# Optimization experiments

Measured on AMD Instinct MI355X. Metric: run time of the kernel, lower is better.

Reference implementation:

```python
import math
import jax, jax.numpy as jnp
import numpy as np

B, S, D = 4, 2048, 1280
H, HD = 16, 80  # num_heads, head_dim
LOG2E = 1.442695041


def setup_inputs() -> dict:
    key = jax.random.key(0)
    ks = jax.random.split(key, 6)
    hidden_states = jax.random.normal(ks[0], (B, S, D), dtype=jnp.float32)
    # additive causal mask: 0 on/below diagonal, large negative above
    causal = jnp.tril(jnp.ones((S, S), dtype=bool))
    attention_mask = jnp.where(causal, 0.0, -1e9).astype(jnp.float32)[None, None, :, :]
    attention_mask = jnp.broadcast_to(attention_mask, (B, 1, S, S))
    scaling = jax.random.normal(ks[1], (HD,), dtype=jnp.float32)
    fan = 1.0 / math.sqrt(D)
    qkv_w = jax.random.normal(ks[2], (3 * H * HD, D), dtype=jnp.float32) * fan
    qkv_b = jax.random.normal(ks[3], (3 * H * HD,), dtype=jnp.float32) * fan
    o_w = jax.random.normal(ks[4], (D, H * HD), dtype=jnp.float32) * (1.0 / math.sqrt(H * HD))
    o_b = jax.random.normal(ks[5], (D,), dtype=jnp.float32) * fan
    return {
        "hidden_states": hidden_states,
        "attention_mask": attention_mask,
        "scaling": scaling,
        "qkv_w": qkv_w,
        "qkv_b": qkv_b,
        "o_w": o_w,
        "o_b": o_b,
    }


def reference(hidden_states, attention_mask, scaling, qkv_w, qkv_b, o_w, o_b):
    b, s, _ = hidden_states.shape
    qkv = hidden_states @ qkv_w.T + qkv_b  # [b, s, 3*H*HD]
    xq, xk, xv = jnp.split(qkv, [H * HD, 2 * H * HD], axis=-1)
    xq = xq.reshape(b, s, H, HD)
    xk = xk.reshape(b, s, H, HD)
    xv = xv.reshape(b, s, H, HD)
    # per-dim query scaling: softplus(scaling) * log2(e) / sqrt(head_dim)
    scale = jax.nn.softplus(scaling) * (LOG2E / math.sqrt(HD))
    xq = xq * scale[None, None, None, :]
    scores = jnp.einsum("bqhd,bkhd->bhqk", xq, xk) + attention_mask  # [b,H,s,s]
    probs = jax.nn.softmax(scores.astype(jnp.float32), axis=-1).astype(xq.dtype)
    out = jnp.einsum("bhqk,bkhd->bqhd", probs, xv).reshape(b, s, H * HD)
    return out @ o_w.T + o_b
```

## Files before the change

kernel.cpp:

```cpp
#include <hip/hip_runtime.h>
#include <math.h>

#define B_ 4
#define S_ 2048
#define D_ 1280
#define H_ 16
#define HD_ 80
#define HHD (H_ * HD_)
#define QKVN (3 * H_ * HD_)

typedef __bf16 bf16x8 __attribute__((ext_vector_type(8)));
typedef __bf16 bf16x4 __attribute__((ext_vector_type(4)));
typedef float  f32x4  __attribute__((ext_vector_type(4)));

__global__ __launch_bounds__(256) void cvt_all(
    const float* __restrict__ h,  __bf16* __restrict__ hb,
    const float* __restrict__ qw, __bf16* __restrict__ qwb,
    const float* __restrict__ ow, __bf16* __restrict__ owb)
{
    const int n0 = (B_ * S_ * D_) / 8;
    const int n1 = (QKVN * D_) / 8;
    const int g = blockIdx.x * 256 + threadIdx.x;

    const float* in;
    __bf16* out;
    int i;
    if (g < n0)            { in = h;  out = hb;  i = g; }
    else if (g < n0 + n1)  { in = qw; out = qwb; i = g - n0; }
    else                   { in = ow; out = owb; i = g - n0 - n1; }

    const float4 a = ((const float4*)in)[2 * (size_t)i];
    const float4 b = ((const float4*)in)[2 * (size_t)i + 1];
    bf16x8 v = {(__bf16)a.x, (__bf16)a.y, (__bf16)a.z, (__bf16)a.w,
                (__bf16)b.x, (__bf16)b.y, (__bf16)b.z, (__bf16)b.w};
    *(bf16x8*)(out + 8 * (size_t)i) = v;
}

__device__ __forceinline__ void async_copy16(const void* g, void* l)
{
    __builtin_amdgcn_global_load_lds(
        (const __attribute__((address_space(1))) unsigned int*)g,
        (__attribute__((address_space(3))) unsigned int*)l, 16, 0, 0);
}

__device__ __forceinline__ bf16x8 frag_ld(const char* lds, int m, int j)
{
    return *(const bf16x8*)(lds + m * 128 + ((j ^ (m & 7)) << 4));
}

__device__ __forceinline__ void stage_half256(
    const __bf16* __restrict__ src, int K, char* ldsmat, int half, int tid)
{
    const int wave = tid >> 6, lane = tid & 63;
#pragma unroll
    for (int i = 0; i < 2; ++i) {
        const int c = (i * 8 + wave) * 64 + lane;
        const int r = half * 128 + (c >> 3);
        const int g = (c & 7) ^ (r & 7);
        async_copy16(src + (size_t)r * K + g * 8,
                     ldsmat + half * 16384 + (i * 8 + wave) * 1024);
    }
}

#define QBAR() do { asm volatile("" ::: "memory");                             \
                    __builtin_amdgcn_s_barrier();                              \
                    __builtin_amdgcn_sched_barrier(0); } while (0)

#define RD_A(MH)                                                               \
    _Pragma("unroll")                                                          \
    for (int mi = 0; mi < 4; ++mi)                                             \
        _Pragma("unroll")                                                      \
        for (int ks = 0; ks < 2; ++ks)                                         \
            af[mi][ks] = frag_ld(lA, wm * 128 + (MH) * 64 + mi * 16 + l16,     \
                                 ks * 4 + quad);
#define RD_B(NH)                                                               \
    _Pragma("unroll")                                                          \
    for (int ni = 0; ni < 2; ++ni)                                             \
        _Pragma("unroll")                                                      \
        for (int ks = 0; ks < 2; ++ks)                                         \
            bfr[ni][ks] = frag_ld(lB, wn * 64 + (NH) * 32 + ni * 16 + l16,     \
                                  ks * 4 + quad);
#define MM16(MH, NH)                                                           \
    __builtin_amdgcn_s_setprio(1);                                             \
    _Pragma("unroll")                                                          \
    for (int mi = 0; mi < 4; ++mi)                                             \
        _Pragma("unroll")                                                      \
        for (int ni = 0; ni < 2; ++ni) {                                       \
            acc[(MH)*4+mi][(NH)*2+ni] = __builtin_amdgcn_mfma_f32_16x16x32_bf16( \
                af[mi][0], bfr[ni][0], acc[(MH)*4+mi][(NH)*2+ni], 0, 0, 0);    \
            acc[(MH)*4+mi][(NH)*2+ni] = __builtin_amdgcn_mfma_f32_16x16x32_bf16( \
                af[mi][1], bfr[ni][1], acc[(MH)*4+mi][(NH)*2+ni], 0, 0, 0);    \
        }                                                                      \
    __builtin_amdgcn_s_setprio(0);

#define GEMM256_PIPELINE(A_, W_)                                               \
    stage_half256(A_, D_, lds[0][0], 0, tid);                                  \
    stage_half256(A_, D_, lds[0][0], 1, tid);                                  \
    stage_half256(W_, D_, lds[0][1], 0, tid);                                  \
    stage_half256(W_, D_, lds[0][1], 1, tid);                                  \
    for (int t = 0; t < nt; ++t) {                                             \
        const int cur = t & 1;                                                 \
        const char* lA = lds[cur][0];                                          \
        const char* lB = lds[cur][1];                                          \
        char* sA = lds[cur ^ 1][0];                                            \
        char* sB = lds[cur ^ 1][1];                                            \
        const int kn = (t + 1 < nt ? t + 1 : t) * 64;                          \
                     \
        stage_half256(A_ + kn, D_, sA, 0, tid);                                \
        asm volatile("s_waitcnt vmcnt(2)" ::: "memory");                       \
        QBAR();                                                                \
        RD_A(0) RD_B(0) MM16(0, 0)                                             \
        stage_half256(A_ + kn, D_, sA, 1, tid);                                \
        RD_B(1) MM16(0, 1)                                                     \
        stage_half256(W_ + kn, D_, sB, 0, tid);                                \
        RD_A(1) RD_B(0) MM16(1, 0)                                             \
        stage_half256(W_ + kn, D_, sB, 1, tid);                                \
        RD_B(1) MM16(1, 1)                                                     \
        QBAR();                                                                \
    }

__global__ __launch_bounds__(512, 2) void gemm_qkv_256(
    const __bf16* __restrict__ Ab, const __bf16* __restrict__ Wb,
    const float* __restrict__ bias, const float* __restrict__ scaling,
    __bf16* __restrict__ Qb, __bf16* __restrict__ Kb, __bf16* __restrict__ Vtb)
{
    __shared__ __align__(16) char lds[2][2][32768];
    const int tid = threadIdx.x;
    const int wave = tid >> 6;
    const int wm = wave >> 2, wn = wave & 3;
    const int l16 = tid & 15, quad = (tid & 63) >> 4;

    const int flat = blockIdx.x;
    const int xcd = flat & 7;
    const int idx = flat >> 3;
    const int m_i = idx & 3, n_g = idx >> 2;
    const int m0 = (xcd * 4 + m_i) * 256;
    const int n0 = n_g * 256;

    const __bf16* A = Ab + (size_t)m0 * D_;
    const __bf16* W = Wb + (size_t)n0 * D_;

    f32x4 acc[8][4];
#pragma unroll
    for (int mi = 0; mi < 8; ++mi)
#pragma unroll
        for (int ni = 0; ni < 4; ++ni) acc[mi][ni] = (f32x4){0.f, 0.f, 0.f, 0.f};

    const int nt = D_ / 64;
    bf16x8 af[4][2], bfr[2][2];

    GEMM256_PIPELINE(A, W)

    const int sec = n_g / 5;
    if (sec == 2) {
#pragma unroll
        for (int ni = 0; ni < 4; ++ni) {
            const int col = n0 + wn * 64 + ni * 16 + l16;
            const int cis = col - 2 * HHD;
            const int h = cis / HD_;
            const int d = cis - h * HD_;
            const float bv = bias[col];
#pragma unroll
            for (int mi = 0; mi < 8; ++mi) {
                const int row0 = m0 + wm * 128 + mi * 16 + quad * 4;
                const int bb = row0 >> 11;
                const int s = row0 & (S_ - 1);
                const size_t bh = (size_t)(bb * H_ + h);
                bf16x4 pv = {(__bf16)(acc[mi][ni][0] + bv),
                             (__bf16)(acc[mi][ni][1] + bv),
                             (__bf16)(acc[mi][ni][2] + bv),
                             (__bf16)(acc[mi][ni][3] + bv)};
                *(bf16x4*)(Vtb + (bh * HD_ + d) * S_ + s) = pv;
            }
        }
    } else {
#pragma unroll
        for (int ni = 0; ni < 4; ++ni) {
            const int col = n0 + wn * 64 + ni * 16 + l16;
            const int cis = col - sec * HHD;
            const int h = cis / HD_;
            const int d = cis - h * HD_;
            const float bv = bias[col];
            float qsv = 0.f;
            if (sec == 0)
                qsv = log1pf(expf(scaling[d])) *
                      (1.442695041f * 1.442695041f / 8.944271910f);
#pragma unroll
            for (int mi = 0; mi < 8; ++mi) {
#pragma unroll
                for (int r = 0; r < 4; ++r) {
                    const int row = m0 + wm * 128 + mi * 16 + quad * 4 + r;
                    const int bb = row >> 11;
                    const int s = row & (S_ - 1);
                    const size_t bh = (size_t)(bb * H_ + h);
                    const float v = acc[mi][ni][r] + bv;
                    if (sec == 0) Qb[(bh * S_ + s) * HD_ + d] = (__bf16)(v * qsv);
                    else          Kb[(bh * S_ + s) * HD_ + d] = (__bf16)v;
                }
            }
        }
    }
}

__global__ __launch_bounds__(512, 2) void gemm_o_256(
    const __bf16* __restrict__ Ab, const __bf16* __restrict__ Wb,
    const float* __restrict__ bias, float* __restrict__ C)
{
    __shared__ __align__(16) char lds[2][2][32768];
    const int tid = threadIdx.x;
    const int wave = tid >> 6;
    const int wm = wave >> 2, wn = wave & 3;
    const int l16 = tid & 15, quad = (tid & 63) >> 4;

    const int flat = blockIdx.x;
    const int xcd = flat & 7;
    const int idx = flat >> 3;
    const int m_i = idx & 3, n_g = idx >> 2;
    const int m0 = (xcd * 4 + m_i) * 256;
    const int n0 = n_g * 256;

    const __bf16* A = Ab + (size_t)m0 * D_;
    const __bf16* W = Wb + (size_t)n0 * D_;

    f32x4 acc[8][4];
#pragma unroll
    for (int mi = 0; mi < 8; ++mi)
#pragma unroll
        for (int ni = 0; ni < 4; ++ni) acc[mi][ni] = (f32x4){0.f, 0.f, 0.f, 0.f};

    const int nt = D_ / 64;
    bf16x8 af[4][2], bfr[2][2];

    GEMM256_PIPELINE(A, W)

#pragma unroll
    for (int ni = 0; ni < 4; ++ni) {
        const int col = n0 + wn * 64 + ni * 16 + l16;
        const float bv = bias[col];
#pragma unroll
        for (int mi = 0; mi < 8; ++mi) {
#pragma unroll
            for (int r = 0; r < 4; ++r) {
                const int row = m0 + wm * 128 + mi * 16 + quad * 4 + r;
                C[(size_t)row * D_ + col] = acc[mi][ni][r] + bv;
            }
        }
    }
}

struct KF8 { bf16x8 f0, f1, f2; };

__device__ __forceinline__ void kload8(
    const __bf16* __restrict__ base, int row, int quad, KF8& kf)
{
    const __bf16* r = base + (size_t)row * HD_;
    kf.f0 = *(const bf16x8*)(r + quad * 8);
    kf.f1 = *(const bf16x8*)(r + 32 + quad * 8);
    bf16x8 z = {};
    if (quad < 2) z = *(const bf16x8*)(r + 64 + quad * 8);
    kf.f2 = z;
}

#define QK3(SREG, KF, QF)                                                      \
    SREG = __builtin_amdgcn_mfma_f32_16x16x32_bf16(KF.f0, QF.f0, SREG, 0, 0, 0); \
    SREG = __builtin_amdgcn_mfma_f32_16x16x32_bf16(KF.f1, QF.f1, SREG, 0, 0, 0); \
    SREG = __builtin_amdgcn_mfma_f32_16x16x32_bf16(KF.f2, QF.f2, SREG, 0, 0, 0);

#define MASK4(SREG, BASE, Q)                                                   \
    _Pragma("unroll")                                                          \
    for (int i = 0; i < 4; ++i)                                                \
        SREG[i] = ((BASE) + quad * 4 + i <= (Q) + l16) ? SREG[i] : -1e30f;

#define ATTN_BODY64(KT)                                                        \
    {                                                                          \
        const int k0 = (KT) * 64;                                              \
        const bool do_lo = ((KT) < nkt_lo);                  \
        const bf16x8 vf00 = *(const bf16x8*)(Vbase + (size_t)( 0 + l16) * S_ + k0 + quad * 8);      \
        const bf16x8 vf01 = *(const bf16x8*)(Vbase + (size_t)( 0 + l16) * S_ + k0 + 32 + quad * 8); \
        const bf16x8 vf10 = *(const bf16x8*)(Vbase + (size_t)(16 + l16) * S_ + k0 + quad * 8);      \
        const bf16x8 vf11 = *(const bf16x8*)(Vbase + (size_t)(16 + l16) * S_ + k0 + 32 + quad * 8); \
        const bf16x8 vf20 = *(const bf16x8*)(Vbase + (size_t)(32 + l16) * S_ + k0 + quad * 8);      \
        const bf16x8 vf21 = *(const bf16x8*)(Vbase + (size_t)(32 + l16) * S_ + k0 + 32 + quad * 8); \
        const bf16x8 vf30 = *(const bf16x8*)(Vbase + (size_t)(48 + l16) * S_ + k0 + quad * 8);      \
        const bf16x8 vf31 = *(const bf16x8*)(Vbase + (size_t)(48 + l16) * S_ + k0 + 32 + quad * 8); \
        const bf16x8 vf40 = *(const bf16x8*)(Vbase + (size_t)(64 + l16) * S_ + k0 + quad * 8);      \
        const bf16x8 vf41 = *(const bf16x8*)(Vbase + (size_t)(64 + l16) * S_ + k0 + 32 + quad * 8); \
        f32x4 sH0 = (f32x4){0.f,0.f,0.f,0.f}, sH1 = sH0, sH2 = sH0, sH3 = sH0; \
        f32x4 sL0 = sH0, sL1 = sH0, sL2 = sH0, sL3 = sH0;                      \
        __builtin_amdgcn_s_setprio(1);                                         \
        QK3(sH0, kf0, qfH) QK3(sH1, kf1, qfH) QK3(sH2, kf2, qfH) QK3(sH3, kf3, qfH) \
        if (do_lo) {                                                           \
            QK3(sL0, kf0, qfL) QK3(sL1, kf1, qfL)                              \
            QK3(sL2, kf2, qfL) QK3(sL3, kf3, qfL)                              \
        }                                                                      \
        __builtin_amdgcn_s_setprio(0);                                         \
        {                                                                      \
            const int kn = ((KT) + 1 < nkt_hi ? (KT) + 1 : (KT)) * 64;         \
            kload8(Kbase, kn + l16, quad, kf0);                                \
            kload8(Kbase, kn + 16 + l16, quad, kf1);                           \
            kload8(Kbase, kn + 32 + l16, quad, kf2);                           \
            kload8(Kbase, kn + 48 + l16, quad, kf3);                           \
        }                                                                      \
        float aH;                                                              \
        {                                                                      \
            if (k0 + 63 > q_hi) {                                              \
                MASK4(sH0, k0, q_hi)      MASK4(sH1, k0 + 16, q_hi)            \
                MASK4(sH2, k0 + 32, q_hi) MASK4(sH3, k0 + 48, q_hi)            \
            }                                                                  \
            float mA = fmaxf(fmaxf(sH0[0], sH0[1]), fmaxf(sH0[2], sH0[3]));    \
            float mB = fmaxf(fmaxf(sH1[0], sH1[1]), fmaxf(sH1[2], sH1[3]));    \
            float mC = fmaxf(fmaxf(sH2[0], sH2[1]), fmaxf(sH2[2], sH2[3]));    \
            float mD = fmaxf(fmaxf(sH3[0], sH3[1]), fmaxf(sH3[2], sH3[3]));    \
            float mx = fmaxf(fmaxf(mA, mB), fmaxf(mC, mD));                    \
            mx = fmaxf(mx, __shfl_xor(mx, 16));                                \
            mx = fmaxf(mx, __shfl_xor(mx, 32));                                \
            const float mn = fmaxf(mH, mx);                                    \
            aH = exp2f(mH - mn);                                               \
            mH = mn;                                                           \
            float rs = 0.f;                                                    \
            _Pragma("unroll")                                                  \
            for (int i = 0; i < 4; ++i) {                                      \
                const float p0 = exp2f(sH0[i] - mn);                           \
                const float p1 = exp2f(sH1[i] - mn);                           \
                const float p2 = exp2f(sH2[i] - mn);                           \
                const float p3 = exp2f(sH3[i] - mn);                           \
                sH0[i] = p0; sH1[i] = p1; sH2[i] = p2; sH3[i] = p3;            \
                rs += (p0 + p1) + (p2 + p3);                                   \
            }                                                                  \
            lH = lH * aH + rs;                                                 \
            *(bf16x4*)&Ps[wave][0][l16][0][quad * 4] =                         \
                (bf16x4){(__bf16)sH0[0], (__bf16)sH0[1], (__bf16)sH0[2], (__bf16)sH0[3]}; \
            *(bf16x4*)&Ps[wave][0][l16][0][16 + quad * 4] =                    \
                (bf16x4){(__bf16)sH1[0], (__bf16)sH1[1], (__bf16)sH1[2], (__bf16)sH1[3]}; \
            *(bf16x4*)&Ps[wave][0][l16][1][quad * 4] =                         \
                (bf16x4){(__bf16)sH2[0], (__bf16)sH2[1], (__bf16)sH2[2], (__bf16)sH2[3]}; \
            *(bf16x4*)&Ps[wave][0][l16][1][16 + quad * 4] =                    \
                (bf16x4){(__bf16)sH3[0], (__bf16)sH3[1], (__bf16)sH3[2], (__bf16)sH3[3]}; \
        }                                                                      \
        float aL = 1.f;                                                        \
        if (do_lo) {                                                           \
            if (k0 + 63 > q_lo) {                                              \
                MASK4(sL0, k0, q_lo)      MASK4(sL1, k0 + 16, q_lo)            \
                MASK4(sL2, k0 + 32, q_lo) MASK4(sL3, k0 + 48, q_lo)            \
            }                                                                  \
            float mA = fmaxf(fmaxf(sL0[0], sL0[1]), fmaxf(sL0[2], sL0[3]));    \
            float mB = fmaxf(fmaxf(sL1[0], sL1[1]), fmaxf(sL1[2], sL1[3]));    \
            float mC = fmaxf(fmaxf(sL2[0], sL2[1]), fmaxf(sL2[2], sL2[3]));    \
            float mD = fmaxf(fmaxf(sL3[0], sL3[1]), fmaxf(sL3[2], sL3[3]));    \
            float mx = fmaxf(fmaxf(mA, mB), fmaxf(mC, mD));                    \
            mx = fmaxf(mx, __shfl_xor(mx, 16));                                \
            mx = fmaxf(mx, __shfl_xor(mx, 32));                                \
            const float mn = fmaxf(mL, mx);                                    \
            aL = exp2f(mL - mn);                                               \
            mL = mn;                                                           \
            float rs = 0.f;                                                    \
            _Pragma("unroll")                                                  \
            for (int i = 0; i < 4; ++i) {                                      \
                const float p0 = exp2f(sL0[i] - mn);                           \
                const float p1 = exp2f(sL1[i] - mn);                           \
                const float p2 = exp2f(sL2[i] - mn);                           \
                const float p3 = exp2f(sL3[i] - mn);                           \
                sL0[i] = p0; sL1[i] = p1; sL2[i] = p2; sL3[i] = p3;            \
                rs += (p0 + p1) + (p2 + p3);                                   \
            }                                                                  \
            lL = lL * aL + rs;                                                 \
            *(bf16x4*)&Ps[wave][1][l16][0][quad * 4] =                         \
                (bf16x4){(__bf16)sL0[0], (__bf16)sL0[1], (__bf16)sL0[2], (__bf16)sL0[3]}; \
            *(bf16x4*)&Ps[wave][1][l16][0][16 + quad * 4] =                    \
                (bf16x4){(__bf16)sL1[0], (__bf16)sL1[1], (__bf16)sL1[2], (__bf16)sL1[3]}; \
            *(bf16x4*)&Ps[wave][1][l16][1][quad * 4] =                         \
                (bf16x4){(__bf16)sL2[0], (__bf16)sL2[1], (__bf16)sL2[2], (__bf16)sL2[3]}; \
            *(bf16x4*)&Ps[wave][1][l16][1][16 + quad * 4] =                    \
                (bf16x4){(__bf16)sL3[0], (__bf16)sL3[1], (__bf16)sL3[2], (__bf16)sL3[3]}; \
        }                                                                      \
        asm volatile("s_waitcnt lgkmcnt(0)" ::: "memory");                     \
        const bf16x8 pfH0 = *(const bf16x8*)&Ps[wave][0][l16][0][quad * 8];    \
        const bf16x8 pfH1 = *(const bf16x8*)&Ps[wave][0][l16][1][quad * 8];    \
        const bf16x8 pfL0 = *(const bf16x8*)&Ps[wave][1][l16][0][quad * 8];    \
        const bf16x8 pfL1 = *(const bf16x8*)&Ps[wave][1][l16][1][quad * 8];    \
        __builtin_amdgcn_s_setprio(1);                                         \
        {                                                                      \
            f32x4 c0, c1, c2, c3, c4;                                          \
            _Pragma("unroll")                                                  \
            for (int i = 0; i < 4; ++i) {                                      \
                c0[i] = oH0[i] * aH; c1[i] = oH1[i] * aH; c2[i] = oH2[i] * aH; \
                c3[i] = oH3[i] * aH; c4[i] = oH4[i] * aH;                      \
            }                                                                  \
            oH0 = __builtin_amdgcn_mfma_f32_16x16x32_bf16(vf00, pfH0, c0, 0, 0, 0); \
            oH1 = __builtin_amdgcn_mfma_f32_16x16x32_bf16(vf10, pfH0, c1, 0, 0, 0); \
            oH2 = __builtin_amdgcn_mfma_f32_16x16x32_bf16(vf20, pfH0, c2, 0, 0, 0); \
            oH3 = __builtin_amdgcn_mfma_f32_16x16x32_bf16(vf30, pfH0, c3, 0, 0, 0); \
            oH4 = __builtin_amdgcn_mfma_f32_16x16x32_bf16(vf40, pfH0, c4, 0, 0, 0); \
            oH0 = __builtin_amdgcn_mfma_f32_16x16x32_bf16(vf01, pfH1, oH0, 0, 0, 0); \
            oH1 = __builtin_amdgcn_mfma_f32_16x16x32_bf16(vf11, pfH1, oH1, 0, 0, 0); \
            oH2 = __builtin_amdgcn_mfma_f32_16x16x32_bf16(vf21, pfH1, oH2, 0, 0, 0); \
            oH3 = __builtin_amdgcn_mfma_f32_16x16x32_bf16(vf31, pfH1, oH3, 0, 0, 0); \
            oH4 = __builtin_amdgcn_mfma_f32_16x16x32_bf16(vf41, pfH1, oH4, 0, 0, 0); \
        }                                                                      \
        if (do_lo) {                                                           \
            f32x4 c0, c1, c2, c3, c4;                                          \
            _Pragma("unroll")                                                  \
            for (int i = 0; i < 4; ++i) {                                      \
                c0[i] = oL0[i] * aL; c1[i] = oL1[i] * aL; c2[i] = oL2[i] * aL; \
                c3[i] = oL3[i] * aL; c4[i] = oL4[i] * aL;                      \
            }                                                                  \
            oL0 = __builtin_amdgcn_mfma_f32_16x16x32_bf16(vf00, pfL0, c0, 0, 0, 0); \
            oL1 = __builtin_amdgcn_mfma_f32_16x16x32_bf16(vf10, pfL0, c1, 0, 0, 0); \
            oL2 = __builtin_amdgcn_mfma_f32_16x16x32_bf16(vf20, pfL0, c2, 0, 0, 0); \
            oL3 = __builtin_amdgcn_mfma_f32_16x16x32_bf16(vf30, pfL0, c3, 0, 0, 0); \
            oL4 = __builtin_amdgcn_mfma_f32_16x16x32_bf16(vf40, pfL0, c4, 0, 0, 0); \
            oL0 = __builtin_amdgcn_mfma_f32_16x16x32_bf16(vf01, pfL1, oL0, 0, 0, 0); \
            oL1 = __builtin_amdgcn_mfma_f32_16x16x32_bf16(vf11, pfL1, oL1, 0, 0, 0); \
            oL2 = __builtin_amdgcn_mfma_f32_16x16x32_bf16(vf21, pfL1, oL2, 0, 0, 0); \
            oL3 = __builtin_amdgcn_mfma_f32_16x16x32_bf16(vf31, pfL1, oL3, 0, 0, 0); \
            oL4 = __builtin_amdgcn_mfma_f32_16x16x32_bf16(vf41, pfL1, oL4, 0, 0, 0); \
        }                                                                      \
        __builtin_amdgcn_s_setprio(0);                                         \
    }

__global__ __launch_bounds__(256, 2) void attn_v13(
    const __bf16* __restrict__ Qb, const __bf16* __restrict__ Kb,
    const __bf16* __restrict__ Vtb, __bf16* __restrict__ out)
{
    __shared__ __align__(16) __bf16 Ps[4][2][16][2][40];

    const int tid = threadIdx.x;
    const int wave = tid >> 6;
    const int lane = tid & 63;
    const int l16 = lane & 15;
    const int quad = lane >> 4;

    const int flat = blockIdx.x;
    const int c = flat & 7;
    const int slot = flat >> 3;
    const int bhgrp = slot >> 4;
    const int xslot = slot & 15;
    const int bh = bhgrp * 8 + c;
    const int x = (xslot + 5 * bhgrp) & 15;
    const int b = bh >> 4, h = bh & 15;

    const int q_lo = 64 * x + 16 * wave;
    const int q_hi = 64 * (31 - x) + 16 * wave;

    const __bf16* Qbase = Qb + (size_t)bh * S_ * HD_;
    const __bf16* Kbase = Kb + (size_t)bh * S_ * HD_;
    const __bf16* Vbase = Vtb + (size_t)bh * HD_ * S_;

    KF8 qfL, qfH;
    kload8(Qbase, q_lo + l16, quad, qfL);
    kload8(Qbase, q_hi + l16, quad, qfH);

    float mL = -1e30f, lL = 0.f, mH = -1e30f, lH = 0.f;
    f32x4 oH0 = (f32x4){0.f,0.f,0.f,0.f}, oH1 = oH0, oH2 = oH0, oH3 = oH0, oH4 = oH0;
    f32x4 oL0 = oH0, oL1 = oH0, oL2 = oH0, oL3 = oH0, oL4 = oH0;

    const int nkt_lo = (q_lo + 16 + 63) >> 6;
    const int nkt_hi = (q_hi + 16 + 63) >> 6;

    KF8 kf0, kf1, kf2, kf3;
    kload8(Kbase, l16, quad, kf0);
    kload8(Kbase, 16 + l16, quad, kf1);
    kload8(Kbase, 32 + l16, quad, kf2);
    kload8(Kbase, 48 + l16, quad, kf3);

    for (int kt = 0; kt < nkt_hi; ++kt) {
        ATTN_BODY64(kt);
    }

    float lHs = lH + __shfl_xor(lH, 16);
    lHs += __shfl_xor(lHs, 32);
    float lLs = lL + __shfl_xor(lL, 16);
    lLs += __shfl_xor(lLs, 32);
    const float invH = 1.f / lHs;
    const float invL = 1.f / lLs;
    const size_t rowH = ((size_t)b * S_ + q_hi + l16) * HHD + h * HD_ + quad * 4;
    const size_t rowL = ((size_t)b * S_ + q_lo + l16) * HHD + h * HD_ + quad * 4;
    {
        bf16x4 v0 = {(__bf16)(oH0[0]*invH), (__bf16)(oH0[1]*invH), (__bf16)(oH0[2]*invH), (__bf16)(oH0[3]*invH)};
        bf16x4 v1 = {(__bf16)(oH1[0]*invH), (__bf16)(oH1[1]*invH), (__bf16)(oH1[2]*invH), (__bf16)(oH1[3]*invH)};
        bf16x4 v2 = {(__bf16)(oH2[0]*invH), (__bf16)(oH2[1]*invH), (__bf16)(oH2[2]*invH), (__bf16)(oH2[3]*invH)};
        bf16x4 v3 = {(__bf16)(oH3[0]*invH), (__bf16)(oH3[1]*invH), (__bf16)(oH3[2]*invH), (__bf16)(oH3[3]*invH)};
        bf16x4 v4 = {(__bf16)(oH4[0]*invH), (__bf16)(oH4[1]*invH), (__bf16)(oH4[2]*invH), (__bf16)(oH4[3]*invH)};
        *(bf16x4*)(out + rowH)      = v0;
        *(bf16x4*)(out + rowH + 16) = v1;
        *(bf16x4*)(out + rowH + 32) = v2;
        *(bf16x4*)(out + rowH + 48) = v3;
        *(bf16x4*)(out + rowH + 64) = v4;
    }
    {
        bf16x4 v0 = {(__bf16)(oL0[0]*invL), (__bf16)(oL0[1]*invL), (__bf16)(oL0[2]*invL), (__bf16)(oL0[3]*invL)};
        bf16x4 v1 = {(__bf16)(oL1[0]*invL), (__bf16)(oL1[1]*invL), (__bf16)(oL1[2]*invL), (__bf16)(oL1[3]*invL)};
        bf16x4 v2 = {(__bf16)(oL2[0]*invL), (__bf16)(oL2[1]*invL), (__bf16)(oL2[2]*invL), (__bf16)(oL2[3]*invL)};
        bf16x4 v3 = {(__bf16)(oL3[0]*invL), (__bf16)(oL3[1]*invL), (__bf16)(oL3[2]*invL), (__bf16)(oL3[3]*invL)};
        bf16x4 v4 = {(__bf16)(oL4[0]*invL), (__bf16)(oL4[1]*invL), (__bf16)(oL4[2]*invL), (__bf16)(oL4[3]*invL)};
        *(bf16x4*)(out + rowL)      = v0;
        *(bf16x4*)(out + rowL + 16) = v1;
        *(bf16x4*)(out + rowL + 32) = v2;
        *(bf16x4*)(out + rowL + 48) = v3;
        *(bf16x4*)(out + rowL + 64) = v4;
    }
}

extern "C" void kernel_launch(void* const* d_in, const int* in_sizes, int n_in,
                              void* d_out, int out_size, void* d_ws, size_t ws_size,
                              hipStream_t stream)
{
    const float* hidden  = (const float*)d_in[0];
    const float* scaling = (const float*)d_in[2];
    const float* qkv_w   = (const float*)d_in[3];
    const float* qkv_b   = (const float*)d_in[4];
    const float* o_w     = (const float*)d_in[5];
    const float* o_b     = (const float*)d_in[6];
    float* out = (float*)d_out;

    const size_t N_HID = (size_t)B_ * S_ * D_;
    const size_t N_QW  = (size_t)QKVN * D_;
    const size_t N_OW  = (size_t)D_ * D_;
    const size_t NPH   = (size_t)B_ * H_ * S_ * HD_;

    __bf16* Ab    = (__bf16*)d_ws;
    __bf16* Wqb   = Ab + N_HID;
    __bf16* Wob   = Wqb + N_QW;
    __bf16* Qb    = Wob + N_OW;
    __bf16* Kb    = Qb + NPH;
    __bf16* Vtb   = Kb + NPH;
    __bf16* attnb = Vtb + NPH;

    const int cvt_blocks = (int)((N_HID + N_QW + N_OW) / 8 / 256);

    cvt_all<<<dim3(cvt_blocks), dim3(256), 0, stream>>>(
        hidden, Ab, qkv_w, Wqb, o_w, Wob);

    gemm_qkv_256<<<dim3(480), dim3(512), 0, stream>>>(
        Ab, Wqb, qkv_b, scaling, Qb, Kb, Vtb);

    attn_v13<<<dim3(16 * H_ * B_), dim3(256), 0, stream>>>(Qb, Kb, Vtb, attnb);

    gemm_o_256<<<dim3(160), dim3(512), 0, stream>>>(
        attnb, Wob, o_b, out);
}
```

Measured before the change: 445.5 us.

## Retile output projection GEMM to 128x128 blocks and raise attention occupancy

Replaces the 256x256-tile output projection GEMM (160 blocks, 512 threads) with a 128x128-tile version (640 blocks, 256 threads) using a new staging helper and a two-half-K double-buffered loop. The goal is to fill all CUs, since 160 blocks underfills a 256-CU device. Separately, the attention kernel's launch bounds minimum blocks per CU goes from 2 to 3, which may cap registers and cause spills. Smaller tiles lower data reuse per block.

```diff
diff --git a/kernel.cpp b/kernel.cpp
--- a/kernel.cpp
+++ b/kernel.cpp
@@ -46,6 +46,19 @@
 __device__ __forceinline__ bf16x8 frag_ld(const char* lds, int m, int j)
 {
     return *(const bf16x8*)(lds + m * 128 + ((j ^ (m & 7)) << 4));
+}
+
+__device__ __forceinline__ void stage128x64(
+    const __bf16* __restrict__ src, int K, char* lds, int tid)
+{
+    const int wave = tid >> 6, lane = tid & 63;
+#pragma unroll
+    for (int i = 0; i < 4; ++i) {
+        const int c = (wave * 4 + i) * 64 + lane;
+        const int r = c >> 3;
+        const int g = (c & 7) ^ (r & 7);
+        async_copy16(src + (size_t)r * K + g * 8, lds + (wave * 4 + i) * 1024);
+    }
 }
 
 __device__ __forceinline__ void stage_half256(
@@ -105,7 +118,6 @@
         char* sA = lds[cur ^ 1][0];                                            \
         char* sB = lds[cur ^ 1][1];                                            \
         const int kn = (t + 1 < nt ? t + 1 : t) * 64;                          \
-                     \
         stage_half256(A_ + kn, D_, sA, 0, tid);                                \
         asm volatile("s_waitcnt vmcnt(2)" ::: "memory");                       \
         QBAR();                                                                \
@@ -202,46 +214,95 @@
     }
 }
 
-__global__ __launch_bounds__(512, 2) void gemm_o_256(
+__global__ __launch_bounds__(256, 2) void gemm_o_128p(
     const __bf16* __restrict__ Ab, const __bf16* __restrict__ Wb,
     const float* __restrict__ bias, float* __restrict__ C)
 {
-    __shared__ __align__(16) char lds[2][2][32768];
+    __shared__ __align__(16) char lds[2][2][16384];
     const int tid = threadIdx.x;
     const int wave = tid >> 6;
-    const int wm = wave >> 2, wn = wave & 3;
+    const int wm = wave >> 1, wn = wave & 1;
     const int l16 = tid & 15, quad = (tid & 63) >> 4;
 
     const int flat = blockIdx.x;
     const int xcd = flat & 7;
     const int idx = flat >> 3;
-    const int m_i = idx & 3, n_g = idx >> 2;
-    const int m0 = (xcd * 4 + m_i) * 256;
-    const int n0 = n_g * 256;
+    const int mm = idx / 10;
+    const int nn = idx - mm * 10;
+    const int m0 = (xcd * 8 + mm) * 128;
+    const int n0 = nn * 128;
 
     const __bf16* A = Ab + (size_t)m0 * D_;
     const __bf16* W = Wb + (size_t)n0 * D_;
 
-    f32x4 acc[8][4];
-#pragma unroll
-    for (int mi = 0; mi < 8; ++mi)
+    f32x4 acc[4][4];
+#pragma unroll
+    for (int mi = 0; mi < 4; ++mi)
 #pragma unroll
         for (int ni = 0; ni < 4; ++ni) acc[mi][ni] = (f32x4){0.f, 0.f, 0.f, 0.f};
 
+    stage128x64(A, D_, lds[0][0], tid);
+    stage128x64(W, D_, lds[0][1], tid);
+
     const int nt = D_ / 64;
-    bf16x8 af[4][2], bfr[2][2];
-
-    GEMM256_PIPELINE(A, W)
+    for (int t = 0; t < nt; ++t) {
+        const int cur = t & 1;
+        const char* lA = lds[cur][0];
+        const char* lB = lds[cur][1];
+        char* sA = lds[cur ^ 1][0];
+        char* sB = lds[cur ^ 1][1];
+        const int kn = (t + 1 < nt ? t + 1 : t) * 64;
+
+        stage128x64(A + kn, D_, sA, tid);
+        asm volatile("s_waitcnt vmcnt(4)" ::: "memory");
+        QBAR();
+        {
+            bf16x8 af[4], bfr[4];
+#pragma unroll
+            for (int mi = 0; mi < 4; ++mi)
+                af[mi] = frag_ld(lA, wm * 64 + mi * 16 + l16, quad);
+#pragma unroll
+            for (int ni = 0; ni < 4; ++ni)
+                bfr[ni] = frag_ld(lB, wn * 64 + ni * 16 + l16, quad);
+            __builtin_amdgcn_s_setprio(1);
+#pragma unroll
+            for (int mi = 0; mi < 4; ++mi)
+#pragma unroll
+                for (int ni = 0; ni < 4; ++ni)
+                    acc[mi][ni] = __builtin_amdgcn_mfma_f32_16x16x32_bf16(
+                        af[mi], bfr[ni], acc[mi][ni], 0, 0, 0);
+            __builtin_amdgcn_s_setprio(0);
+        }
+        stage128x64(W + kn, D_, sB, tid);
+        {
+            bf16x8 af[4], bfr[4];
+#pragma unroll
+            for (int mi = 0; mi < 4; ++mi)
+                af[mi] = frag_ld(lA, wm * 64 + mi * 16 + l16, 4 + quad);
+#pragma unroll
+            for (int ni = 0; ni < 4; ++ni)
+                bfr[ni] = frag_ld(lB, wn * 64 + ni * 16 + l16, 4 + quad);
+            __builtin_amdgcn_s_setprio(1);
+#pragma unroll
+            for (int mi = 0; mi < 4; ++mi)
+#pragma unroll
+                for (int ni = 0; ni < 4; ++ni)
+                    acc[mi][ni] = __builtin_amdgcn_mfma_f32_16x16x32_bf16(
+                        af[mi], bfr[ni], acc[mi][ni], 0, 0, 0);
+            __builtin_amdgcn_s_setprio(0);
+        }
+        QBAR();
+    }
 
 #pragma unroll
     for (int ni = 0; ni < 4; ++ni) {
         const int col = n0 + wn * 64 + ni * 16 + l16;
         const float bv = bias[col];
 #pragma unroll
-        for (int mi = 0; mi < 8; ++mi) {
+        for (int mi = 0; mi < 4; ++mi) {
 #pragma unroll
             for (int r = 0; r < 4; ++r) {
-                const int row = m0 + wm * 128 + mi * 16 + quad * 4 + r;
+                const int row = m0 + wm * 64 + mi * 16 + quad * 4 + r;
                 C[(size_t)row * D_ + col] = acc[mi][ni][r] + bv;
             }
         }
@@ -418,7 +479,7 @@
         __builtin_amdgcn_s_setprio(0);                                         \
     }
 
-__global__ __launch_bounds__(256, 2) void attn_v13(
+__global__ __launch_bounds__(256, 3) void attn_v13(
     const __bf16* __restrict__ Qb, const __bf16* __restrict__ Kb,
     const __bf16* __restrict__ Vtb, __bf16* __restrict__ out)
 {
@@ -536,6 +597,6 @@
 
     attn_v13<<<dim3(16 * H_ * B_), dim3(256), 0, stream>>>(Qb, Kb, Vtb, attnb);
 
-    gemm_o_256<<<dim3(160), dim3(512), 0, stream>>>(
+    gemm_o_128p<<<dim3(640), dim3(256), 0, stream>>>(
         attnb, Wob, o_b, out);
 }
```

Measured after the change: 664.2 us. +49.1%, slower.
